# Optimization experiments

Hardware: AMD Instinct MI355X
Metric: run time of the kernel (lower is better)

The kernel has to match this reference:

```python
import jax, jax.numpy as jnp
import numpy as np

B, T, E = 4, 2048, 1024
H, D = 16, 64  # num_heads, head_size; H*D == E


def setup_inputs() -> dict:
    key = jax.random.key(0)
    ks = jax.random.split(key, 8)
    s = 0.02
    x = jax.random.normal(ks[0], (B, T, E), dtype=jnp.float32)
    attention_mask = jnp.ones((B, T), dtype=jnp.float32)
    # stacked per-head projection weights (no bias), torch Linear: y = x @ W.T
    Wq = jax.random.normal(ks[1], (H, E, D), dtype=jnp.float32) * s
    Wk = jax.random.normal(ks[2], (H, E, D), dtype=jnp.float32) * s
    Wv = jax.random.normal(ks[3], (H, E, D), dtype=jnp.float32) * s
    Wo = jax.random.normal(ks[4], (E, E), dtype=jnp.float32) * s
    bo = jnp.zeros((E,), dtype=jnp.float32)
    return {"x": x, "attention_mask": attention_mask, "Wq": Wq, "Wk": Wk,
            "Wv": Wv, "Wo": Wo, "bo": bo}


def reference(x, attention_mask, Wq, Wk, Wv, Wo, bo):
    # per-head projections, vectorized over heads: [B,T,E] x [H,E,D] -> [B,H,T,D]
    q = jnp.einsum('bte,hed->bhtd', x, Wq)
    k = jnp.einsum('bte,hed->bhtd', x, Wk)
    v = jnp.einsum('bte,hed->bhtd', x, Wv)
    scores = jnp.einsum('bhtd,bhsd->bhts', q, k) / jnp.sqrt(jnp.float32(D))
    # causal mask (tril): masked_fill with -inf
    causal = jnp.tril(jnp.ones((T, T), dtype=bool))
    scores = jnp.where(causal[None, None, :, :], scores, -jnp.inf)
    # padding mask: weights += (1 - mask) * finfo(float32).min, broadcast over queries
    neg = jnp.finfo(jnp.float32).min
    scores = scores + ((1.0 - attention_mask) * neg)[:, None, None, :]
    weights = jax.nn.softmax(scores, axis=-1)
    out = jnp.einsum('bhts,bhsd->bthd', weights, v).reshape(B, T, H * D)
    return out @ Wo.T + bo
```

## Files before the change

kernel.cpp:

```cpp
#include <hip/hip_runtime.h>
#include <hip/hip_bf16.h>

#define B_ 4
#define T_ 2048
#define E_ 1024
#define H_ 16
#define D_ 64
#define M_ (B_*T_)

typedef short bf16x8 __attribute__((ext_vector_type(8)));
typedef float f32x4  __attribute__((ext_vector_type(4)));
typedef float f32x16 __attribute__((ext_vector_type(16)));

__device__ __forceinline__ short f2bf(float f) {
    __hip_bfloat16 h = __float2bfloat16(f);
    return *reinterpret_cast<short*>(&h);
}

__device__ __forceinline__ unsigned int pk2(float a, float b) {
    unsigned int ua = __float_as_uint(a), ub = __float_as_uint(b);
    return ((ua + 0x8000u) >> 16) | ((ub + 0x8000u) & 0xffff0000u);
}

__device__ __forceinline__ void async_ld16(const void* g, void* l) {
    __builtin_amdgcn_global_load_lds(
        (const __attribute__((address_space(1))) unsigned int*)g,
        (__attribute__((address_space(3))) unsigned int*)l, 16, 0, 0);
}

__global__ void conv_bf16(const float* __restrict__ src, short* __restrict__ dst) {
    const int i = blockIdx.x * 256 + threadIdx.x;
    float4 v = ((const float4*)src)[i];
    short4 o = make_short4(f2bf(v.x), f2bf(v.y), f2bf(v.z), f2bf(v.w));
    ((short4*)dst)[i] = o;
}

__global__ void bias_prep(const float* __restrict__ mask, float* __restrict__ bias) {
    const int i = blockIdx.x * 256 + threadIdx.x;
    float bm = (1.0f - mask[i]) * -3.402823466e38f;
    bias[i] = fmaf(bm, 1.4426950f, -8.6561700f);
}

__global__ void wtrans(const float* __restrict__ Wq,
                       const float* __restrict__ Wk,
                       const float* __restrict__ Wv,
                       short* __restrict__ Wt) {
    const int which = blockIdx.z;
    const float* __restrict__ W = (which == 0) ? Wq : (which == 1) ? Wk : Wv;
    const int h  = blockIdx.y;
    const int e0 = blockIdx.x * 64;

    __shared__ float tile[64][65];
    const int tid = threadIdx.x;

#pragma unroll
    for (int r = 0; r < 4; ++r) {
        int lin = tid + r * 256;
        int er = lin >> 4, c4 = (lin & 15) * 4;
        float4 v = *(const float4*)(W + ((size_t)h * E_ + e0 + er) * D_ + c4);
        tile[er][c4 + 0] = v.x; tile[er][c4 + 1] = v.y;
        tile[er][c4 + 2] = v.z; tile[er][c4 + 3] = v.w;
    }
    __syncthreads();
#pragma unroll
    for (int r = 0; r < 4; ++r) {
        int lin = tid + r * 256;
        int dr = lin >> 4, j4 = (lin & 15) * 4;
        short4 o = make_short4(f2bf(tile[j4 + 0][dr]), f2bf(tile[j4 + 1][dr]),
                               f2bf(tile[j4 + 2][dr]), f2bf(tile[j4 + 3][dr]));
        *(short4*)(Wt + ((size_t)which * 1024 + h * 64 + dr) * E_ + e0 + j4) = o;
    }
}

template <int MODE>
__global__ __launch_bounds__(256) void mfma_gemm(
        const short* __restrict__ A,
        const short* __restrict__ Bt,
        short* __restrict__ qo, short* __restrict__ ko, short* __restrict__ vo,
        float* __restrict__ Cout, const float* __restrict__ bo) {
    __shared__ __align__(16) short As[128 * 32];
    __shared__ __align__(16) short Bs[128 * 32];

    const int tid  = threadIdx.x;
    const int wave = tid >> 6, lane = tid & 63;
    const int c = lane & 15, quad = lane >> 4;
    const int wm = wave >> 1, wn = wave & 1;
    const int m0 = blockIdx.x * 128;
    const int n0 = blockIdx.y * 128;

    int rowS[2], kgS[2];
#pragma unroll
    for (int r = 0; r < 2; ++r) {
        int p = r * 256 + wave * 64 + lane;
        rowS[r] = p >> 2;
        kgS[r]  = (p & 3) ^ ((rowS[r] >> 1) & 3);
    }

    f32x4 acc[4][4] = {};

    for (int k0 = 0; k0 < 1024; k0 += 32) {
#pragma unroll
        for (int r = 0; r < 2; ++r) {
            async_ld16(A  + (size_t)(m0 + rowS[r]) * 1024 + k0 + kgS[r] * 8,
                       As + (r * 256 + wave * 64) * 8);
            async_ld16(Bt + (size_t)(n0 + rowS[r]) * 1024 + k0 + kgS[r] * 8,
                       Bs + (r * 256 + wave * 64) * 8);
        }
        __syncthreads();

        bf16x8 af[4], bf[4];
#pragma unroll
        for (int mi = 0; mi < 4; ++mi) {
            int row = wm * 64 + mi * 16 + c;
            int pos = row * 4 + (quad ^ ((row >> 1) & 3));
            af[mi] = *(const bf16x8*)(As + pos * 8);
        }
#pragma unroll
        for (int ni = 0; ni < 4; ++ni) {
            int row = wn * 64 + ni * 16 + c;
            int pos = row * 4 + (quad ^ ((row >> 1) & 3));
            bf[ni] = *(const bf16x8*)(Bs + pos * 8);
        }
#pragma unroll
        for (int mi = 0; mi < 4; ++mi)
#pragma unroll
            for (int ni = 0; ni < 4; ++ni)
                acc[mi][ni] = __builtin_amdgcn_mfma_f32_16x16x32_bf16(
                    af[mi], bf[ni], acc[mi][ni], 0, 0, 0);
        __syncthreads();
    }

    if (MODE == 0) {
        const int which = n0 >> 10;
        const int nb = n0 & 1023;
        if (which == 2) {
#pragma unroll
            for (int mi = 0; mi < 4; ++mi) {
                const int m = m0 + wm * 64 + mi * 16 + quad * 4;
                const int b = m >> 11, t = m & 2047;
#pragma unroll
                for (int ni = 0; ni < 4; ++ni) {
                    const int n = nb + wn * 64 + ni * 16 + c;
                    const int h = n >> 6, d = n & 63;
                    short4 s4 = make_short4(f2bf(acc[mi][ni][0]), f2bf(acc[mi][ni][1]),
                                            f2bf(acc[mi][ni][2]), f2bf(acc[mi][ni][3]));
                    *(short4*)(vo + (((size_t)b * H_ + h) * D_ + d) * T_ + t) = s4;
                }
            }
        } else {
            short* __restrict__ outp = (which == 0) ? qo : ko;
            const float sc = (which == 0) ? 0.18033688f : 1.0f;
#pragma unroll
            for (int mi = 0; mi < 4; ++mi) {
#pragma unroll
                for (int i = 0; i < 4; ++i) {
                    const int m = m0 + wm * 64 + mi * 16 + quad * 4 + i;
                    const int b = m >> 11, t = m & 2047;
#pragma unroll
                    for (int ni = 0; ni < 4; ++ni) {
                        const int n = nb + wn * 64 + ni * 16 + c;
                        const int h = n >> 6, d = n & 63;
                        outp[(((size_t)b * H_ + h) * T_ + t) * D_ + d] =
                            f2bf(acc[mi][ni][i] * sc);
                    }
                }
            }
        }
    } else {
#pragma unroll
        for (int mi = 0; mi < 4; ++mi) {
#pragma unroll
            for (int i = 0; i < 4; ++i) {
                const int m = m0 + wm * 64 + mi * 16 + quad * 4 + i;
#pragma unroll
                for (int ni = 0; ni < 4; ++ni) {
                    const int n = n0 + wn * 64 + ni * 16 + c;
                    Cout[(size_t)m * E_ + n] = acc[mi][ni][i] + bo[n];
                }
            }
        }
    }
}

__global__ __launch_bounds__(256) void flash_attn5(
        const short* __restrict__ qg,
        const short* __restrict__ kg,
        const short* __restrict__ vtg,
        const float* __restrict__ biasg,
        short* __restrict__ attn) {
    const int h = blockIdx.x, b = blockIdx.y;
    const int z = blockIdx.z;
    const int tid  = threadIdx.x;
    const int wave = tid >> 6, lane = tid & 63;
    const int ln = lane & 31, hi = lane >> 5;

    __shared__ __align__(16) char lds[25088];

    const size_t bh = (size_t)b * H_ + h;
    const short* qbh  = qg  + bh * (size_t)T_ * D_;
    const short* kbh  = kg  + bh * (size_t)T_ * D_;
    const short* vtbh = vtg + bh * (size_t)D_ * T_;
    const float* biasb = biasg + (size_t)b * T_;

    const int ks = tid >> 3, kgs = (tid & 7) ^ (ks & 7);
    const int vd = tid >> 2, vgs = ((tid & 3) - ((tid >> 3) & 3)) & 3;

    int kaddr[4];
#pragma unroll
    for (int kc = 0; kc < 4; ++kc)
        kaddr[kc] = ln * 128 + ((((kc << 1) + hi) ^ (ln & 7)) << 4);
    int vaddr[4];
#pragma unroll
    for (int dh = 0; dh < 2; ++dh)
#pragma unroll
        for (int kc2 = 0; kc2 < 2; ++kc2) {
            int d = dh * 32 + ln;
            vaddr[dh * 2 + kc2] =
                4096 + d * 64 + (((((kc2 << 1) + hi) + (d >> 1)) & 3) << 4);
        }

#pragma unroll
    for (int r = 0; r < 2; ++r)
        async_ld16(biasb + 4 * (r * 256 + wave * 64 + lane),
                   lds + 16384 + r * 4096 + wave * 1024);

#define STAGE_T(s0v, boff) do {                                             \
        async_ld16(kbh + (size_t)((s0v) + ks) * D_ + (kgs << 3),            \
                   lds + (boff) + wave * 1024);                             \
        async_ld16(vtbh + (size_t)vd * T_ + (s0v) + (vgs << 3),             \
                   lds + (boff) + 4096 + wave * 1024);                      \
    } while (0)

#pragma unroll 1
    for (int sidx = 0; sidx < 2; ++sidx) {
        const int kblk = sidx ? z : (15 - z);
        const int q0w = kblk * 128 + wave * 32;
        const int mytile = 4 * kblk + wave;
        const int nt = 4 * kblk + 4;

        bf16x8 qf[4];
#pragma unroll
        for (int kc = 0; kc < 4; ++kc)
            qf[kc] = *(const bf16x8*)(qbh + (size_t)(q0w + ln) * D_ + kc * 16 + hi * 8);

        f32x16 O0 = {}, O1 = {};
        float lacc = 0.0f;

        STAGE_T(0, 0);
        int bufoff = 0;
        for (int tt = 0; tt < nt; ++tt) {
            if (tt + 1 < nt) {
                STAGE_T((tt + 1) << 5, bufoff ^ 8192);
                asm volatile("s_waitcnt vmcnt(2)" ::: "memory");
            } else {
                asm volatile("s_waitcnt vmcnt(0)" ::: "memory");
            }
            __builtin_amdgcn_s_barrier();

            if (tt <= mytile) {
                const int s0 = tt << 5;

                f32x4 b4[4];
#pragma unroll
                for (int g = 0; g < 4; ++g)
                    b4[g] = *(const f32x4*)(lds + 16384 + (s0 + g * 8 + hi * 4) * 4);

                f32x16 S = {};
#pragma unroll
                for (int kc = 0; kc < 4; ++kc) {
                    bf16x8 ka = *(const bf16x8*)(lds + bufoff + kaddr[kc]);
                    S = __builtin_amdgcn_mfma_f32_32x32x16_bf16(ka, qf[kc], S, 0, 0, 0);
                }

                float p[16];
#pragma unroll
                for (int r = 0; r < 16; ++r) {
                    float bb = ((const float*)&b4[r >> 2])[r & 3];
                    p[r] = __builtin_amdgcn_exp2f(S[r] + bb);
                }
                if (tt == mytile) {
#pragma unroll
                    for (int r = 0; r < 16; ++r)
                        if (((r & 3) + ((r >> 2) << 3) + (hi << 2)) > ln)
                            p[r] = 0.0f;
                }
                {
                    float t0 = (p[0] + p[1]) + (p[2] + p[3]);
                    float t1 = (p[4] + p[5]) + (p[6] + p[7]);
                    float t2 = (p[8] + p[9]) + (p[10] + p[11]);
                    float t3 = (p[12] + p[13]) + (p[14] + p[15]);
                    lacc += (t0 + t1) + (t2 + t3);
                }

                unsigned int u0 = pk2(p[0], p[1]),  u1 = pk2(p[2], p[3]);
                unsigned int u2 = pk2(p[4], p[5]),  u3 = pk2(p[6], p[7]);
                unsigned int u4 = pk2(p[8], p[9]),  u5 = pk2(p[10], p[11]);
                unsigned int u6 = pk2(p[12], p[13]), u7 = pk2(p[14], p[15]);
                asm("v_permlane32_swap_b32 %0, %1" : "+v"(u0), "+v"(u2));
                asm("v_permlane32_swap_b32 %0, %1" : "+v"(u1), "+v"(u3));
                asm("v_permlane32_swap_b32 %0, %1" : "+v"(u4), "+v"(u6));
                asm("v_permlane32_swap_b32 %0, %1" : "+v"(u5), "+v"(u7));
                union { unsigned int w[4]; bf16x8 v; } pa0, pa1;
                pa0.w[0] = u0; pa0.w[1] = u1; pa0.w[2] = u2; pa0.w[3] = u3;
                pa1.w[0] = u4; pa1.w[1] = u5; pa1.w[2] = u6; pa1.w[3] = u7;

                bf16x8 v00 = *(const bf16x8*)(lds + bufoff + vaddr[0]);
                bf16x8 v01 = *(const bf16x8*)(lds + bufoff + vaddr[1]);
                O0 = __builtin_amdgcn_mfma_f32_32x32x16_bf16(pa0.v, v00, O0, 0, 0, 0);
                O0 = __builtin_amdgcn_mfma_f32_32x32x16_bf16(pa1.v, v01, O0, 0, 0, 0);
                bf16x8 v10 = *(const bf16x8*)(lds + bufoff + vaddr[2]);
                bf16x8 v11 = *(const bf16x8*)(lds + bufoff + vaddr[3]);
                O1 = __builtin_amdgcn_mfma_f32_32x32x16_bf16(pa0.v, v10, O1, 0, 0, 0);
                O1 = __builtin_amdgcn_mfma_f32_32x32x16_bf16(pa1.v, v11, O1, 0, 0, 0);
            }

            __builtin_amdgcn_s_barrier();
            bufoff ^= 8192;
        }

        unsigned int la = __float_as_uint(lacc), lb2 = la;
        asm("v_permlane32_swap_b32 %0, %1" : "+v"(la), "+v"(lb2));
        const float ltot = __uint_as_float(la) + __uint_as_float(lb2);

        float* lsh = (float*)(lds + 24576) + wave * 32;
        if (hi == 0) lsh[ln] = 1.0f / ltot;
        __syncthreads();

        short* ab = attn + (size_t)b * T_ * E_ + h * D_;
#pragma unroll
        for (int r = 0; r < 16; ++r) {
            const int qrow = (r & 3) + ((r >> 2) << 3) + (hi << 2);
            const float iv = lsh[qrow];
            const size_t base = (size_t)(q0w + qrow) * E_;
            ab[base + ln]      = f2bf(O0[r] * iv);
            ab[base + 32 + ln] = f2bf(O1[r] * iv);
        }
    }
#undef STAGE_T
}

extern "C" void kernel_launch(void* const* d_in, const int* in_sizes, int n_in,
                              void* d_out, int out_size, void* d_ws, size_t ws_size,
                              hipStream_t stream) {
    const float* x    = (const float*)d_in[0];
    const float* mask = (const float*)d_in[1];
    const float* Wq   = (const float*)d_in[2];
    const float* Wk   = (const float*)d_in[3];
    const float* Wv   = (const float*)d_in[4];
    const float* Wo   = (const float*)d_in[5];
    const float* bo   = (const float*)d_in[6];
    float* out        = (float*)d_out;

    const size_t S = (size_t)M_ * E_;
    char* ws = (char*)d_ws;
    short* xb   = (short*)ws;
    short* qb   = (short*)(ws + S * 2);
    short* kb   = (short*)(ws + S * 4);
    short* vtb  = (short*)(ws + S * 6);
    short* Wt   = (short*)(ws + S * 8);
    short* Wob  = (short*)(ws + S * 8 + (size_t)3 * 1024 * 1024 * 2);
    float* bias = (float*)(ws + S * 8 + (size_t)4 * 1024 * 1024 * 2);
    short* attnb = xb;

    conv_bf16<<<dim3(M_ * E_ / 1024), 256, 0, stream>>>(x, xb);
    conv_bf16<<<dim3(E_ * E_ / 1024), 256, 0, stream>>>(Wo, Wob);
    wtrans<<<dim3(E_ / 64, H_, 3), 256, 0, stream>>>(Wq, Wk, Wv, Wt);
    bias_prep<<<dim3(B_ * T_ / 256), 256, 0, stream>>>(mask, bias);

    mfma_gemm<0><<<dim3(M_ / 128, 3 * E_ / 128), 256, 0, stream>>>(
        xb, Wt, qb, kb, vtb, nullptr, nullptr);

    flash_attn5<<<dim3(H_, B_, 8), 256, 0, stream>>>(qb, kb, vtb, bias, attnb);

    mfma_gemm<1><<<dim3(M_ / 128, E_ / 128), 256, 0, stream>>>(
        attnb, Wob, nullptr, nullptr, nullptr, out, bo);
}
```

Before: 270.1 us.

## Widen flash attention to 8 waves with 4-slot ring and deeper prefetch

The attention kernel moves to 512-thread blocks. Each block now handles 256 query rows from a single query block, instead of a balanced pair of 128-row blocks. K/V staging uses a 4-slot LDS ring with a two-tile prefetch distance, and the trailing per-iteration barrier is dropped. Half the threads load K and half load V^T. Other changes: s_setprio is raised around the MFMA groups, and the manual bf16 pack is replaced by v_cvt_pk_bf16_f32. The aim is more overlap of loads with compute and better MFMA issue, at the risk of load imbalance across causal blocks and higher LDS use per block.

Result: faster. 256.5 us (-5.1%).

```diff
diff --git a/kernel.cpp b/kernel.cpp
--- a/kernel.cpp
+++ b/kernel.cpp
@@ -15,11 +15,6 @@
 __device__ __forceinline__ short f2bf(float f) {
     __hip_bfloat16 h = __float2bfloat16(f);
     return *reinterpret_cast<short*>(&h);
-}
-
-__device__ __forceinline__ unsigned int pk2(float a, float b) {
-    unsigned int ua = __float_as_uint(a), ub = __float_as_uint(b);
-    return ((ua + 0x8000u) >> 16) | ((ub + 0x8000u) & 0xffff0000u);
 }
 
 __device__ __forceinline__ void async_ld16(const void* g, void* l) {
@@ -182,19 +177,22 @@
     }
 }
 
-__global__ __launch_bounds__(256) void flash_attn5(
+__global__ __launch_bounds__(512, 4) void flash_attn6(
         const short* __restrict__ qg,
         const short* __restrict__ kg,
         const short* __restrict__ vtg,
         const float* __restrict__ biasg,
         short* __restrict__ attn) {
     const int h = blockIdx.x, b = blockIdx.y;
-    const int z = blockIdx.z;
+    const int kb = 7 - blockIdx.z;
     const int tid  = threadIdx.x;
     const int wave = tid >> 6, lane = tid & 63;
     const int ln = lane & 31, hi = lane >> 5;
-
-    __shared__ __align__(16) char lds[25088];
+    const int q0w = kb * 256 + wave * 32;
+    const int mytile = 8 * kb + wave;
+    const int nt = 8 * kb + 8;
+
+    __shared__ __align__(16) char lds[41984];
 
     const size_t bh = (size_t)b * H_ + h;
     const short* qbh  = qg  + bh * (size_t)T_ * D_;
@@ -202,8 +200,10 @@
     const short* vtbh = vtg + bh * (size_t)D_ * T_;
     const float* biasb = biasg + (size_t)b * T_;
 
-    const int ks = tid >> 3, kgs = (tid & 7) ^ (ks & 7);
-    const int vd = tid >> 2, vgs = ((tid & 3) - ((tid >> 3) & 3)) & 3;
+    const bool stK = (tid < 256);
+    const int t2 = tid & 255;
+    const int ks = t2 >> 3, kgs = (t2 & 7) ^ (ks & 7);
+    const int vd = t2 >> 2, vgs = ((t2 & 3) - (vd >> 1)) & 3;
 
     int kaddr[4];
 #pragma unroll
@@ -219,124 +219,122 @@
                 4096 + d * 64 + (((((kc2 << 1) + hi) + (d >> 1)) & 3) << 4);
         }
 
-#pragma unroll
-    for (int r = 0; r < 2; ++r)
-        async_ld16(biasb + 4 * (r * 256 + wave * 64 + lane),
-                   lds + 16384 + r * 4096 + wave * 1024);
-
-#define STAGE_T(s0v, boff) do {                                             \
-        async_ld16(kbh + (size_t)((s0v) + ks) * D_ + (kgs << 3),            \
-                   lds + (boff) + wave * 1024);                             \
-        async_ld16(vtbh + (size_t)vd * T_ + (s0v) + (vgs << 3),             \
-                   lds + (boff) + 4096 + wave * 1024);                      \
+    bf16x8 qf[4];
+#pragma unroll
+    for (int kc = 0; kc < 4; ++kc)
+        qf[kc] = *(const bf16x8*)(qbh + (size_t)(q0w + ln) * D_ + kc * 16 + hi * 8);
+
+    async_ld16(biasb + ((wave << 6) + lane) * 4, lds + 32768 + wave * 1024);
+
+#define STAGE_T(tt2) do {                                                   \
+        const int _s0 = (tt2) << 5;                                         \
+        const int _bb = ((tt2) & 3) * 8192;                                 \
+        if (stK) async_ld16(kbh + (size_t)(_s0 + ks) * D_ + (kgs << 3),     \
+                            lds + _bb + (wave & 3) * 1024);                 \
+        else     async_ld16(vtbh + (size_t)vd * T_ + _s0 + (vgs << 3),      \
+                            lds + _bb + 4096 + (wave & 3) * 1024);          \
     } while (0)
 
-#pragma unroll 1
-    for (int sidx = 0; sidx < 2; ++sidx) {
-        const int kblk = sidx ? z : (15 - z);
-        const int q0w = kblk * 128 + wave * 32;
-        const int mytile = 4 * kblk + wave;
-        const int nt = 4 * kblk + 4;
-
-        bf16x8 qf[4];
-#pragma unroll
-        for (int kc = 0; kc < 4; ++kc)
-            qf[kc] = *(const bf16x8*)(qbh + (size_t)(q0w + ln) * D_ + kc * 16 + hi * 8);
-
-        f32x16 O0 = {}, O1 = {};
-        float lacc = 0.0f;
-
-        STAGE_T(0, 0);
-        int bufoff = 0;
-        for (int tt = 0; tt < nt; ++tt) {
-            if (tt + 1 < nt) {
-                STAGE_T((tt + 1) << 5, bufoff ^ 8192);
-                asm volatile("s_waitcnt vmcnt(2)" ::: "memory");
-            } else {
-                asm volatile("s_waitcnt vmcnt(0)" ::: "memory");
-            }
-            __builtin_amdgcn_s_barrier();
-
-            if (tt <= mytile) {
-                const int s0 = tt << 5;
-
-                f32x4 b4[4];
-#pragma unroll
-                for (int g = 0; g < 4; ++g)
-                    b4[g] = *(const f32x4*)(lds + 16384 + (s0 + g * 8 + hi * 4) * 4);
-
-                f32x16 S = {};
-#pragma unroll
-                for (int kc = 0; kc < 4; ++kc) {
-                    bf16x8 ka = *(const bf16x8*)(lds + bufoff + kaddr[kc]);
-                    S = __builtin_amdgcn_mfma_f32_32x32x16_bf16(ka, qf[kc], S, 0, 0, 0);
-                }
-
-                float p[16];
-#pragma unroll
-                for (int r = 0; r < 16; ++r) {
-                    float bb = ((const float*)&b4[r >> 2])[r & 3];
-                    p[r] = __builtin_amdgcn_exp2f(S[r] + bb);
-                }
-                if (tt == mytile) {
-#pragma unroll
-                    for (int r = 0; r < 16; ++r)
-                        if (((r & 3) + ((r >> 2) << 3) + (hi << 2)) > ln)
-                            p[r] = 0.0f;
-                }
-                {
-                    float t0 = (p[0] + p[1]) + (p[2] + p[3]);
-                    float t1 = (p[4] + p[5]) + (p[6] + p[7]);
-                    float t2 = (p[8] + p[9]) + (p[10] + p[11]);
-                    float t3 = (p[12] + p[13]) + (p[14] + p[15]);
-                    lacc += (t0 + t1) + (t2 + t3);
-                }
-
-                unsigned int u0 = pk2(p[0], p[1]),  u1 = pk2(p[2], p[3]);
-                unsigned int u2 = pk2(p[4], p[5]),  u3 = pk2(p[6], p[7]);
-                unsigned int u4 = pk2(p[8], p[9]),  u5 = pk2(p[10], p[11]);
-                unsigned int u6 = pk2(p[12], p[13]), u7 = pk2(p[14], p[15]);
-                asm("v_permlane32_swap_b32 %0, %1" : "+v"(u0), "+v"(u2));
-                asm("v_permlane32_swap_b32 %0, %1" : "+v"(u1), "+v"(u3));
-                asm("v_permlane32_swap_b32 %0, %1" : "+v"(u4), "+v"(u6));
-                asm("v_permlane32_swap_b32 %0, %1" : "+v"(u5), "+v"(u7));
-                union { unsigned int w[4]; bf16x8 v; } pa0, pa1;
-                pa0.w[0] = u0; pa0.w[1] = u1; pa0.w[2] = u2; pa0.w[3] = u3;
-                pa1.w[0] = u4; pa1.w[1] = u5; pa1.w[2] = u6; pa1.w[3] = u7;
-
-                bf16x8 v00 = *(const bf16x8*)(lds + bufoff + vaddr[0]);
-                bf16x8 v01 = *(const bf16x8*)(lds + bufoff + vaddr[1]);
-                O0 = __builtin_amdgcn_mfma_f32_32x32x16_bf16(pa0.v, v00, O0, 0, 0, 0);
-                O0 = __builtin_amdgcn_mfma_f32_32x32x16_bf16(pa1.v, v01, O0, 0, 0, 0);
-                bf16x8 v10 = *(const bf16x8*)(lds + bufoff + vaddr[2]);
-                bf16x8 v11 = *(const bf16x8*)(lds + bufoff + vaddr[3]);
-                O1 = __builtin_amdgcn_mfma_f32_32x32x16_bf16(pa0.v, v10, O1, 0, 0, 0);
-                O1 = __builtin_amdgcn_mfma_f32_32x32x16_bf16(pa1.v, v11, O1, 0, 0, 0);
-            }
-
-            __builtin_amdgcn_s_barrier();
-            bufoff ^= 8192;
-        }
-
-        unsigned int la = __float_as_uint(lacc), lb2 = la;
-        asm("v_permlane32_swap_b32 %0, %1" : "+v"(la), "+v"(lb2));
-        const float ltot = __uint_as_float(la) + __uint_as_float(lb2);
-
-        float* lsh = (float*)(lds + 24576) + wave * 32;
-        if (hi == 0) lsh[ln] = 1.0f / ltot;
-        __syncthreads();
-
-        short* ab = attn + (size_t)b * T_ * E_ + h * D_;
-#pragma unroll
-        for (int r = 0; r < 16; ++r) {
-            const int qrow = (r & 3) + ((r >> 2) << 3) + (hi << 2);
-            const float iv = lsh[qrow];
-            const size_t base = (size_t)(q0w + qrow) * E_;
-            ab[base + ln]      = f2bf(O0[r] * iv);
-            ab[base + 32 + ln] = f2bf(O1[r] * iv);
+    STAGE_T(0);
+    STAGE_T(1);
+
+    f32x16 O0 = {}, O1 = {};
+    float lacc = 0.0f;
+
+    for (int tt = 0; tt < nt; ++tt) {
+        if (tt + 2 < nt) STAGE_T(tt + 2);
+        const int rem = nt - 1 - tt;
+        if (rem >= 2)      asm volatile("s_waitcnt vmcnt(2)" ::: "memory");
+        else if (rem == 1) asm volatile("s_waitcnt vmcnt(1)" ::: "memory");
+        else               asm volatile("s_waitcnt vmcnt(0)" ::: "memory");
+        __builtin_amdgcn_s_barrier();
+
+        if (tt <= mytile) {
+            const int s0 = tt << 5;
+            const int bb = (tt & 3) * 8192;
+
+            f32x4 b4[4];
+#pragma unroll
+            for (int g = 0; g < 4; ++g)
+                b4[g] = *(const f32x4*)(lds + 32768 + (s0 + g * 8 + hi * 4) * 4);
+
+            f32x16 S = {};
+            __builtin_amdgcn_s_setprio(1);
+#pragma unroll
+            for (int kc = 0; kc < 4; ++kc) {
+                bf16x8 ka = *(const bf16x8*)(lds + bb + kaddr[kc]);
+                S = __builtin_amdgcn_mfma_f32_32x32x16_bf16(ka, qf[kc], S, 0, 0, 0);
+            }
+            __builtin_amdgcn_s_setprio(0);
+
+            float p[16];
+#pragma unroll
+            for (int r = 0; r < 16; ++r) {
+                float bb2 = ((const float*)&b4[r >> 2])[r & 3];
+                p[r] = __builtin_amdgcn_exp2f(S[r] + bb2);
+            }
+            if (tt == mytile) {
+#pragma unroll
+                for (int r = 0; r < 16; ++r)
+                    if (((r & 3) + ((r >> 2) << 3) + (hi << 2)) > ln)
+                        p[r] = 0.0f;
+            }
+            {
+                float t0 = (p[0] + p[1]) + (p[2] + p[3]);
+                float t1 = (p[4] + p[5]) + (p[6] + p[7]);
+                float t2s = (p[8] + p[9]) + (p[10] + p[11]);
+                float t3 = (p[12] + p[13]) + (p[14] + p[15]);
+                lacc += (t0 + t1) + (t2s + t3);
+            }
+
+            unsigned int u0, u1, u2, u3, u4, u5, u6, u7;
+            asm("v_cvt_pk_bf16_f32 %0, %1, %2" : "=v"(u0) : "v"(p[0]),  "v"(p[1]));
+            asm("v_cvt_pk_bf16_f32 %0, %1, %2" : "=v"(u1) : "v"(p[2]),  "v"(p[3]));
+            asm("v_cvt_pk_bf16_f32 %0, %1, %2" : "=v"(u2) : "v"(p[4]),  "v"(p[5]));
+            asm("v_cvt_pk_bf16_f32 %0, %1, %2" : "=v"(u3) : "v"(p[6]),  "v"(p[7]));
+            asm("v_cvt_pk_bf16_f32 %0, %1, %2" : "=v"(u4) : "v"(p[8]),  "v"(p[9]));
+            asm("v_cvt_pk_bf16_f32 %0, %1, %2" : "=v"(u5) : "v"(p[10]), "v"(p[11]));
+            asm("v_cvt_pk_bf16_f32 %0, %1, %2" : "=v"(u6) : "v"(p[12]), "v"(p[13]));
+            asm("v_cvt_pk_bf16_f32 %0, %1, %2" : "=v"(u7) : "v"(p[14]), "v"(p[15]));
+            asm("v_permlane32_swap_b32 %0, %1" : "+v"(u0), "+v"(u2));
+            asm("v_permlane32_swap_b32 %0, %1" : "+v"(u1), "+v"(u3));
+            asm("v_permlane32_swap_b32 %0, %1" : "+v"(u4), "+v"(u6));
+            asm("v_permlane32_swap_b32 %0, %1" : "+v"(u5), "+v"(u7));
+            union { unsigned int w[4]; bf16x8 v; } pa0, pa1;
+            pa0.w[0] = u0; pa0.w[1] = u1; pa0.w[2] = u2; pa0.w[3] = u3;
+            pa1.w[0] = u4; pa1.w[1] = u5; pa1.w[2] = u6; pa1.w[3] = u7;
+
+            bf16x8 v00 = *(const bf16x8*)(lds + bb + vaddr[0]);
+            bf16x8 v01 = *(const bf16x8*)(lds + bb + vaddr[1]);
+            bf16x8 v10 = *(const bf16x8*)(lds + bb + vaddr[2]);
+            bf16x8 v11 = *(const bf16x8*)(lds + bb + vaddr[3]);
+            __builtin_amdgcn_s_setprio(1);
+            O0 = __builtin_amdgcn_mfma_f32_32x32x16_bf16(pa0.v, v00, O0, 0, 0, 0);
+            O0 = __builtin_amdgcn_mfma_f32_32x32x16_bf16(pa1.v, v01, O0, 0, 0, 0);
+            O1 = __builtin_amdgcn_mfma_f32_32x32x16_bf16(pa0.v, v10, O1, 0, 0, 0);
+            O1 = __builtin_amdgcn_mfma_f32_32x32x16_bf16(pa1.v, v11, O1, 0, 0, 0);
+            __builtin_amdgcn_s_setprio(0);
         }
     }
 #undef STAGE_T
+
+    unsigned int la = __float_as_uint(lacc), lb2 = la;
+    asm("v_permlane32_swap_b32 %0, %1" : "+v"(la), "+v"(lb2));
+    const float ltot = __uint_as_float(la) + __uint_as_float(lb2);
+
+    float* lsh = (float*)(lds + 40960) + wave * 32;
+    if (hi == 0) lsh[ln] = 1.0f / ltot;
+    __syncthreads();
+
+    short* ab = attn + (size_t)b * T_ * E_ + h * D_;
+#pragma unroll
+    for (int r = 0; r < 16; ++r) {
+        const int qrow = (r & 3) + ((r >> 2) << 3) + (hi << 2);
+        const float iv = lsh[qrow];
+        const size_t base = (size_t)(q0w + qrow) * E_;
+        ab[base + ln]      = f2bf(O0[r] * iv);
+        ab[base + 32 + ln] = f2bf(O1[r] * iv);
+    }
 }
 
 extern "C" void kernel_launch(void* const* d_in, const int* in_sizes, int n_in,
@@ -370,7 +368,7 @@
     mfma_gemm<0><<<dim3(M_ / 128, 3 * E_ / 128), 256, 0, stream>>>(
         xb, Wt, qb, kb, vtb, nullptr, nullptr);
 
-    flash_attn5<<<dim3(H_, B_, 8), 256, 0, stream>>>(qb, kb, vtb, bias, attnb);
+    flash_attn6<<<dim3(H_, B_, 8), 512, 0, stream>>>(qb, kb, vtb, bias, attnb);
 
     mfma_gemm<1><<<dim3(M_ / 128, E_ / 128), 256, 0, stream>>>(
         attnb, Wob, nullptr, nullptr, nullptr, out, bo);
```
